# Optimization experiments

Hardware: AMD Instinct MI355X
Metric: run time of the kernel (lower is better)

The kernel has to match this reference:

```python
import jax, jax.numpy as jnp
import numpy as np
from functools import partial

N_NODES = 100000
N_EDGES = 3200000
F_IN, H1, H2, C_OUT = 128, 64, 32, 2


def setup_inputs() -> dict:
    key = jax.random.key(0)
    ks = jax.random.split(key, 8)
    x = jax.random.normal(ks[0], (N_NODES, F_IN), dtype=jnp.float32)
    edge_index = jax.random.randint(ks[1], (2, N_EDGES), 0, N_NODES, dtype=jnp.int64)
    def glorot(k, fan_in, fan_out):
        s = jnp.sqrt(6.0 / (fan_in + fan_out))
        return jax.random.uniform(k, (fan_in, fan_out), jnp.float32, -s, s)
    return {
        "x": x,
        "edge_index": edge_index,
        "W1": glorot(ks[2], F_IN, H1), "b1": jnp.zeros((H1,), jnp.float32),
        "W2": glorot(ks[3], H1, H2),   "b2": jnp.zeros((H2,), jnp.float32),
        "W3": glorot(ks[4], H2, C_OUT), "b3": jnp.zeros((C_OUT,), jnp.float32),
    }


def _gcn_norm(edge_index, num_nodes):
    # add self-loops, compute symmetric normalization D^{-1/2} (A+I) D^{-1/2}
    loop = jnp.arange(num_nodes, dtype=edge_index.dtype)
    src = jnp.concatenate([edge_index[0], loop])
    dst = jnp.concatenate([edge_index[1], loop])
    deg = jax.ops.segment_sum(jnp.ones_like(dst, dtype=jnp.float32), dst,
                              num_segments=num_nodes)
    dinv = jax.lax.rsqrt(deg)  # deg >= 1 because of self-loops
    norm = dinv[src] * dinv[dst]  # [E + N]
    return src, dst, norm


def _gcn_conv(x, W, b, src, dst, norm, num_nodes):
    # PyG GCNConv: linear transform, then normalized scatter-aggregate, then bias
    xw = x @ W                                   # [N, F_out]
    msg = xw[src] * norm[:, None]                # [E+N, F_out] gather + scale
    out = jax.ops.segment_sum(msg, dst, num_segments=num_nodes)
    return out + b


def reference(x, edge_index, W1, b1, W2, b2, W3, b3):
    n = x.shape[0]
    src, dst, norm = _gcn_norm(edge_index, n)
    h = jax.nn.relu(_gcn_conv(x, W1, b1, src, dst, norm, n))
    # dropout is identity in eval mode
    h = jax.nn.relu(_gcn_conv(h, W2, b2, src, dst, norm, n))
    h = _gcn_conv(h, W3, b3, src, dst, norm, n)
    return jax.nn.log_softmax(h, axis=1)
```

## Files before the change

### kernel.cpp

```cpp
#include <hip/hip_runtime.h>
#include <hip/hip_bf16.h>
#include <math.h>

constexpr int N = 100000;
constexpr int E = 3200000;
constexpr int FIN = 128, H1 = 64, H2 = 32, COUT = 2;

constexpr int BUK_SHIFT = 6;
constexpr int BUK_NODES = 64;
constexpr int NBUK = (N + BUK_NODES - 1) / BUK_NODES;
constexpr int CAP = 2560;
constexpr int SEG_SHIFT = 14;
constexpr int NSEG = 7;
constexpr int KEYS = BUK_NODES * NSEG;
constexpr int RP_STR = BUK_NODES + 1;

constexpr int MS_TPB = 1024;
constexpr int MS_EPT = 24;
constexpr int CHUNK = MS_TPB * MS_EPT;
constexpr int MS_WGS = (E + CHUNK - 1) / CHUNK;

__global__ void k_initcur(int* __restrict__ gcursor) {
    int i = blockIdx.x * blockDim.x + threadIdx.x;
    if (i < NBUK) gcursor[i] = i * CAP;
}

__global__ __launch_bounds__(MS_TPB)
void k_mslice(const int* __restrict__ src, const int* __restrict__ dst,
              int* __restrict__ gcursor, unsigned* __restrict__ ebuf) {
    __shared__ int cnt[NBUK];
    __shared__ int base[NBUK];
    const int t = threadIdx.x;
    for (int i = t; i < NBUK; i += MS_TPB) cnt[i] = 0;
    __syncthreads();
    const int e0 = blockIdx.x * CHUNK;

    int rb[MS_EPT];
    unsigned rv[MS_EPT];
#pragma unroll
    for (int j = 0; j < MS_EPT; ++j) {
        int e = e0 + j * MS_TPB + t;
        if (e < E) {
            int d = dst[e];
            int b = d >> BUK_SHIFT;
            rb[j] = b;
            rv[j] = (unsigned)src[e] | ((unsigned)(d & (BUK_NODES - 1)) << 17);
            atomicAdd(&cnt[b], 1);
        } else {
            rb[j] = -1; rv[j] = 0;
        }
    }
    __syncthreads();
    for (int i = t; i < NBUK; i += MS_TPB) {
        int c = cnt[i];
        base[i] = c ? atomicAdd(&gcursor[i], c) : 0;
    }
    __syncthreads();
    for (int i = t; i < NBUK; i += MS_TPB) cnt[i] = 0;
    __syncthreads();
#pragma unroll
    for (int j = 0; j < MS_EPT; ++j) {
        int b = rb[j];
        if (b >= 0) {
            int r = atomicAdd(&cnt[b], 1);
            int p = base[b] + r;
            if (p < (b + 1) * CAP) ebuf[p] = rv[j];
        }
    }
}

__global__ __launch_bounds__(256)
void k_build(const int* __restrict__ gcursor, unsigned* __restrict__ ebuf,
             int* __restrict__ rp, float* __restrict__ dinv) {
    __shared__ unsigned ent[CAP];
    __shared__ int cnt[512];
    __shared__ int sa[512];
    __shared__ int sb[512];
    __shared__ int cur[512];
    const int b = blockIdx.x;
    const int t = threadIdx.x;
    int fill = gcursor[b] - b * CAP;
    if (fill > CAP) fill = CAP;
    const int gbase = b * CAP;

    cnt[t] = 0; cnt[t + 256] = 0;
    __syncthreads();
    for (int j = t; j < fill; j += 256) {
        unsigned v = ebuf[gbase + j];
        ent[j] = v;
        int key = (int)(v >> 17) * NSEG + (int)((v & 0x1FFFFu) >> SEG_SHIFT);
        atomicAdd(&cnt[key], 1);
    }
    __syncthreads();
    sa[t] = cnt[t]; sa[t + 256] = cnt[t + 256];
    __syncthreads();
    int* pin = sa; int* pout = sb;
    for (int off = 1; off < 512; off <<= 1) {
        pout[t]       = pin[t]       + ((t >= off)       ? pin[t - off]       : 0);
        pout[t + 256] = pin[t + 256] + ((t + 256 >= off) ? pin[t + 256 - off] : 0);
        __syncthreads();
        int* tmp = pin; pin = pout; pout = tmp;
    }
    {
        int ex0 = pin[t] - cnt[t];
        int ex1 = pin[t + 256] - cnt[t + 256];
        cur[t] = gbase + ex0;
        cur[t + 256] = gbase + ex1;
        if (t < KEYS && (t % NSEG) == 0)
            rp[b * RP_STR + t / NSEG] = gbase + ex0;
        int k2 = t + 256;
        if (k2 < KEYS && (k2 % NSEG) == 0)
            rp[b * RP_STR + k2 / NSEG] = gbase + ex1;
        if (t == 0) rp[b * RP_STR + BUK_NODES] = gbase + fill;
    }
    if (t < BUK_NODES) {
        int deg = 0;
#pragma unroll
        for (int s = 0; s < NSEG; ++s) deg += cnt[t * NSEG + s];
        int node = (b << BUK_SHIFT) + t;
        if (node < N) dinv[node] = rsqrtf((float)deg + 1.0f);
    }
    __syncthreads();
    for (int j = t; j < fill; j += 256) {
        unsigned v = ent[j];
        int key = (int)(v >> 17) * NSEG + (int)((v & 0x1FFFFu) >> SEG_SHIFT);
        int p = atomicAdd(&cur[key], 1);
        ebuf[p] = v & 0x1FFFFu;
    }
}

template<int FI, int FO>
__global__ __launch_bounds__(256)
void k_gemm_tile_bf(const float* __restrict__ h, const float* __restrict__ Wg,
                    const float* __restrict__ dinv, __hip_bfloat16* __restrict__ y) {
    constexpr int TX  = FO / 4;
    constexpr int TY  = 256 / TX;
    constexpr int RPT = 64 / TY;
    constexpr int XS  = 68;
    constexpr int KQ  = FI / 4;

    __shared__ float xsT[FI][XS];

    const int tid = threadIdx.x;
    const int tx = tid % TX;
    const int ty = tid / TX;
    const int row0 = blockIdx.x * 64;

    for (int idx = tid; idx < 64 * KQ; idx += 256) {
        int g   = idx / 8;
        int rlo = idx % 8;
        int k4  = g % KQ;
        int rhi = g / KQ;
        int r   = rlo + 8 * rhi;
        int row = row0 + r;
        float4 v = make_float4(0.f, 0.f, 0.f, 0.f);
        if (row < N) v = *(const float4*)(h + (size_t)row * FI + 4 * k4);
        xsT[4 * k4 + 0][r] = v.x;
        xsT[4 * k4 + 1][r] = v.y;
        xsT[4 * k4 + 2][r] = v.z;
        xsT[4 * k4 + 3][r] = v.w;
    }
    __syncthreads();

    float acc[RPT][4];
#pragma unroll
    for (int i = 0; i < RPT; ++i)
#pragma unroll
        for (int c = 0; c < 4; ++c) acc[i][c] = 0.0f;

#pragma unroll 4
    for (int k = 0; k < FI; ++k) {
        const float4 wv = *(const float4*)(Wg + (size_t)k * FO + 4 * tx);
        float xv[RPT];
        if constexpr (RPT == 4) {
            float4 t = *(const float4*)&xsT[k][4 * ty];
            xv[0] = t.x; xv[1] = t.y; xv[2] = t.z; xv[3] = t.w;
        } else {
            float2 t = *(const float2*)&xsT[k][2 * ty];
            xv[0] = t.x; xv[1] = t.y;
        }
#pragma unroll
        for (int i = 0; i < RPT; ++i) {
            acc[i][0] = fmaf(xv[i], wv.x, acc[i][0]);
            acc[i][1] = fmaf(xv[i], wv.y, acc[i][1]);
            acc[i][2] = fmaf(xv[i], wv.z, acc[i][2]);
            acc[i][3] = fmaf(xv[i], wv.w, acc[i][3]);
        }
    }

#pragma unroll
    for (int i = 0; i < RPT; ++i) {
        int row = row0 + ty * RPT + i;
        if (row >= N) continue;
        float di = dinv[row];
        auto cvt = [](float f) -> unsigned short {
            __hip_bfloat16 b = __float2bfloat16(f);
            return *reinterpret_cast<unsigned short*>(&b);
        };
        ushort4 pk;
        pk.x = cvt(di * acc[i][0]);
        pk.y = cvt(di * acc[i][1]);
        pk.z = cvt(di * acc[i][2]);
        pk.w = cvt(di * acc[i][3]);
        *(ushort4*)&y[(size_t)row * FO + 4 * tx] = pk;
    }
}

template<int FI, int FO, int ROWS>
__global__ __launch_bounds__(FO * ROWS)
void k_gemm_scale(const float* __restrict__ h, const float* __restrict__ W,
                  const float* __restrict__ dinv, float* __restrict__ y) {
    __shared__ float xs[ROWS][FI];
    const int j = threadIdx.x;
    const int r = threadIdx.y;
    const int row0 = blockIdx.x * ROWS;
    const int tid = r * FO + j;
    constexpr int NT = FO * ROWS;
    for (int t = tid; t < ROWS * FI; t += NT) {
        int rr = t / FI, kk = t % FI;
        int row = row0 + rr;
        xs[rr][kk] = (row < N) ? h[(size_t)row * FI + kk] : 0.0f;
    }
    __syncthreads();
    const int row = row0 + r;
    if (row >= N) return;
    float acc = 0.0f;
#pragma unroll
    for (int k = 0; k < FI; ++k)
        acc = fmaf(xs[r][k], W[k * FO + j], acc);
    y[(size_t)row * FO + j] = dinv[row] * acc;
}

template<int F, bool RELU>
__global__ __launch_bounds__(256)
void k_aggregate_bf(const int* __restrict__ rp, const unsigned* __restrict__ csr,
                    const __hip_bfloat16* __restrict__ y, const float* __restrict__ dinv,
                    const float* __restrict__ b, float* __restrict__ out) {
    constexpr int LPN = F / 2;
    constexpr int NPB = 256 / LPN;
    const int fp = threadIdx.x;
    const int n = blockIdx.x * NPB + threadIdx.y;
    if (n >= N) return;
    const unsigned* yw = (const unsigned*)y;

    auto load2 = [&](int s) -> float2 {
        unsigned u = yw[(size_t)s * LPN + fp];
        float2 v;
        v.x = __uint_as_float(u << 16);
        v.y = __uint_as_float(u & 0xffff0000u);
        return v;
    };

    const int rb = (n >> BUK_SHIFT) * RP_STR + (n & (BUK_NODES - 1));
    const int j0 = rp[rb], j1 = rp[rb + 1];
    float2 acc = load2(n);
    int j = j0;
    for (; j + 8 <= j1; j += 8) {
        int s0 = (int)csr[j],     s1 = (int)csr[j + 1], s2 = (int)csr[j + 2], s3 = (int)csr[j + 3];
        int s4 = (int)csr[j + 4], s5 = (int)csr[j + 5], s6 = (int)csr[j + 6], s7 = (int)csr[j + 7];
        float2 v0 = load2(s0), v1 = load2(s1), v2 = load2(s2), v3 = load2(s3);
        float2 v4 = load2(s4), v5 = load2(s5), v6 = load2(s6), v7 = load2(s7);
        acc.x += ((v0.x + v1.x) + (v2.x + v3.x)) + ((v4.x + v5.x) + (v6.x + v7.x));
        acc.y += ((v0.y + v1.y) + (v2.y + v3.y)) + ((v4.y + v5.y) + (v6.y + v7.y));
    }
    for (; j < j1; ++j) {
        float2 v = load2((int)csr[j]);
        acc.x += v.x; acc.y += v.y;
    }
    const float di = dinv[n];
    float o0 = fmaf(di, acc.x, b[2 * fp]);
    float o1 = fmaf(di, acc.y, b[2 * fp + 1]);
    if (RELU) { o0 = fmaxf(o0, 0.0f); o1 = fmaxf(o1, 0.0f); }
    float2 res; res.x = o0; res.y = o1;
    *(float2*)&out[(size_t)n * F + 2 * fp] = res;
}

__global__ __launch_bounds__(256)
void k_final(const int* __restrict__ rp, const unsigned* __restrict__ csr,
             const float* __restrict__ y, const float* __restrict__ dinv,
             const float* __restrict__ bias, float* __restrict__ out) {
    const int c = threadIdx.x;
    const int n = blockIdx.x * 128 + threadIdx.y;
    float z = 0.0f;
    if (n < N) {
        const int rb = (n >> BUK_SHIFT) * RP_STR + (n & (BUK_NODES - 1));
        int j = rp[rb];
        const int j1 = rp[rb + 1];
        float acc = y[2 * n + c];
        for (; j + 4 <= j1; j += 4) {
            int s0 = (int)csr[j], s1 = (int)csr[j + 1], s2 = (int)csr[j + 2], s3 = (int)csr[j + 3];
            float a0 = y[2 * s0 + c], a1 = y[2 * s1 + c];
            float a2 = y[2 * s2 + c], a3 = y[2 * s3 + c];
            acc += (a0 + a1) + (a2 + a3);
        }
        for (; j < j1; ++j) acc += y[2 * (int)csr[j] + c];
        z = fmaf(dinv[n], acc, bias[c]);
    }
    float zo = __shfl_xor(z, 1);
    if (n < N) {
        float m = fmaxf(z, zo);
        float lse = m + logf(expf(z - m) + expf(zo - m));
        out[2 * n + c] = z - lse;
    }
}

extern "C" void kernel_launch(void* const* d_in, const int* in_sizes, int n_in,
                              void* d_out, int out_size, void* d_ws, size_t ws_size,
                              hipStream_t stream) {
    const float* x   = (const float*)d_in[0];
    const int*   ei  = (const int*)d_in[1];
    const float* W1  = (const float*)d_in[2];
    const float* b1  = (const float*)d_in[3];
    const float* W2  = (const float*)d_in[4];
    const float* b2  = (const float*)d_in[5];
    const float* W3  = (const float*)d_in[6];
    const float* b3  = (const float*)d_in[7];
    float* out = (float*)d_out;

    const int* src = ei;
    const int* dst = ei + E;

    char* p = (char*)d_ws;
    float*    dinv    = (float*)p;    p += (size_t)N * 4;
    int*      gcursor = (int*)p;      p += (size_t)NBUK * 4;
    int*      rp      = (int*)p;      p += (size_t)NBUK * RP_STR * 4;
    unsigned* ebuf    = (unsigned*)p; p += (size_t)NBUK * CAP * 4;
    char*     bufA    = p;            p += (size_t)N * 64 * 4;
    char*     bufB    = p;            p += (size_t)N * 64 * 4;

    __hip_bfloat16* y1 = (__hip_bfloat16*)bufA;
    float*          h1 = (float*)bufB;
    __hip_bfloat16* y2 = (__hip_bfloat16*)bufA;
    float*          h2 = (float*)(bufA + (size_t)N * H2 * 2);
    float*          y3 = (float*)bufB;

    k_initcur<<<(NBUK + 255) / 256, 256, 0, stream>>>(gcursor);
    k_mslice <<<MS_WGS, MS_TPB, 0, stream>>>(src, dst, gcursor, ebuf);
    k_build  <<<NBUK, 256, 0, stream>>>(gcursor, ebuf, rp, dinv);

    k_gemm_tile_bf<FIN, H1><<<(N + 63) / 64, 256, 0, stream>>>(x, W1, dinv, y1);
    k_aggregate_bf<H1, true><<<(N + 7) / 8, dim3(32, 8), 0, stream>>>(rp, ebuf, y1, dinv, b1, h1);

    k_gemm_tile_bf<H1, H2><<<(N + 63) / 64, 256, 0, stream>>>(h1, W2, dinv, y2);
    k_aggregate_bf<H2, true><<<(N + 15) / 16, dim3(16, 16), 0, stream>>>(rp, ebuf, y2, dinv, b2, h2);

    k_gemm_scale<H2, COUT, 128><<<(N + 127) / 128, dim3(COUT, 128), 0, stream>>>(h2, W3, dinv, y3);
    k_final<<<(N + 127) / 128, dim3(2, 128), 0, stream>>>(rp, ebuf, y3, dinv, b3, out);
}
```

Measured before the change: 379.2 us.

## Use persistent aggregation grids, finer source segments, and memset cursor init

The aggregation kernels now run as a fixed-size persistent grid that loops over node groups, replacing one block per group. The CSR build sorts each bucket's edges into 13 source segments of 8K nodes instead of 7 of 16K, which changes the gather order for better locality, and it widens the local histogram and scan to 1024 bins. The per-bucket cursor-initialization kernel is replaced by a memset, with cursors now relative offsets. The costs are a longer scan in the build step and the loop overhead of a grid-stride loop.

```diff
diff --git a/kernel.cpp b/kernel.cpp
--- a/kernel.cpp
+++ b/kernel.cpp
@@ -10,9 +10,10 @@
 constexpr int BUK_NODES = 64;
 constexpr int NBUK = (N + BUK_NODES - 1) / BUK_NODES;
 constexpr int CAP = 2560;
-constexpr int SEG_SHIFT = 14;
-constexpr int NSEG = 7;
+constexpr int SEG_SHIFT = 13;
+constexpr int NSEG = 13;
 constexpr int KEYS = BUK_NODES * NSEG;
+constexpr int BINS = 1024;
 constexpr int RP_STR = BUK_NODES + 1;
 
 constexpr int MS_TPB = 1024;
@@ -20,10 +21,7 @@
 constexpr int CHUNK = MS_TPB * MS_EPT;
 constexpr int MS_WGS = (E + CHUNK - 1) / CHUNK;
 
-__global__ void k_initcur(int* __restrict__ gcursor) {
-    int i = blockIdx.x * blockDim.x + threadIdx.x;
-    if (i < NBUK) gcursor[i] = i * CAP;
-}
+constexpr int PERS_BLKS = 1536;
 
 __global__ __launch_bounds__(MS_TPB)
 void k_mslice(const int* __restrict__ src, const int* __restrict__ dst,
@@ -64,7 +62,7 @@
         if (b >= 0) {
             int r = atomicAdd(&cnt[b], 1);
             int p = base[b] + r;
-            if (p < (b + 1) * CAP) ebuf[p] = rv[j];
+            if (p < CAP) ebuf[(size_t)b * CAP + p] = rv[j];
         }
     }
 }
@@ -73,17 +71,18 @@
 void k_build(const int* __restrict__ gcursor, unsigned* __restrict__ ebuf,
              int* __restrict__ rp, float* __restrict__ dinv) {
     __shared__ unsigned ent[CAP];
-    __shared__ int cnt[512];
-    __shared__ int sa[512];
-    __shared__ int sb[512];
-    __shared__ int cur[512];
+    __shared__ int cnt[BINS];
+    __shared__ int sa[BINS];
+    __shared__ int sb[BINS];
+    __shared__ int cur[BINS];
     const int b = blockIdx.x;
     const int t = threadIdx.x;
-    int fill = gcursor[b] - b * CAP;
+    int fill = gcursor[b];
     if (fill > CAP) fill = CAP;
     const int gbase = b * CAP;
 
-    cnt[t] = 0; cnt[t + 256] = 0;
+#pragma unroll
+    for (int q = 0; q < 4; ++q) cnt[t + 256 * q] = 0;
     __syncthreads();
     for (int j = t; j < fill; j += 256) {
         unsigned v = ebuf[gbase + j];
@@ -92,27 +91,28 @@
         atomicAdd(&cnt[key], 1);
     }
     __syncthreads();
-    sa[t] = cnt[t]; sa[t + 256] = cnt[t + 256];
+#pragma unroll
+    for (int q = 0; q < 4; ++q) sa[t + 256 * q] = cnt[t + 256 * q];
     __syncthreads();
     int* pin = sa; int* pout = sb;
-    for (int off = 1; off < 512; off <<= 1) {
-        pout[t]       = pin[t]       + ((t >= off)       ? pin[t - off]       : 0);
-        pout[t + 256] = pin[t + 256] + ((t + 256 >= off) ? pin[t + 256 - off] : 0);
+    for (int off = 1; off < BINS; off <<= 1) {
+#pragma unroll
+        for (int q = 0; q < 4; ++q) {
+            int idx = t + 256 * q;
+            pout[idx] = pin[idx] + ((idx >= off) ? pin[idx - off] : 0);
+        }
         __syncthreads();
         int* tmp = pin; pin = pout; pout = tmp;
     }
-    {
-        int ex0 = pin[t] - cnt[t];
-        int ex1 = pin[t + 256] - cnt[t + 256];
-        cur[t] = gbase + ex0;
-        cur[t + 256] = gbase + ex1;
-        if (t < KEYS && (t % NSEG) == 0)
-            rp[b * RP_STR + t / NSEG] = gbase + ex0;
-        int k2 = t + 256;
-        if (k2 < KEYS && (k2 % NSEG) == 0)
-            rp[b * RP_STR + k2 / NSEG] = gbase + ex1;
-        if (t == 0) rp[b * RP_STR + BUK_NODES] = gbase + fill;
-    }
+#pragma unroll
+    for (int q = 0; q < 4; ++q) {
+        int idx = t + 256 * q;
+        int ex = pin[idx] - cnt[idx];
+        cur[idx] = gbase + ex;
+        if (idx < KEYS && (idx % NSEG) == 0)
+            rp[b * RP_STR + idx / NSEG] = gbase + ex;
+    }
+    if (t == 0) rp[b * RP_STR + BUK_NODES] = gbase + fill;
     if (t < BUK_NODES) {
         int deg = 0;
 #pragma unroll
@@ -238,9 +238,8 @@
                     const float* __restrict__ b, float* __restrict__ out) {
     constexpr int LPN = F / 2;
     constexpr int NPB = 256 / LPN;
+    constexpr int NGRP = (N + NPB - 1) / NPB;
     const int fp = threadIdx.x;
-    const int n = blockIdx.x * NPB + threadIdx.y;
-    if (n >= N) return;
     const unsigned* yw = (const unsigned*)y;
 
     auto load2 = [&](int s) -> float2 {
@@ -251,28 +250,32 @@
         return v;
     };
 
-    const int rb = (n >> BUK_SHIFT) * RP_STR + (n & (BUK_NODES - 1));
-    const int j0 = rp[rb], j1 = rp[rb + 1];
-    float2 acc = load2(n);
-    int j = j0;
-    for (; j + 8 <= j1; j += 8) {
-        int s0 = (int)csr[j],     s1 = (int)csr[j + 1], s2 = (int)csr[j + 2], s3 = (int)csr[j + 3];
-        int s4 = (int)csr[j + 4], s5 = (int)csr[j + 5], s6 = (int)csr[j + 6], s7 = (int)csr[j + 7];
-        float2 v0 = load2(s0), v1 = load2(s1), v2 = load2(s2), v3 = load2(s3);
-        float2 v4 = load2(s4), v5 = load2(s5), v6 = load2(s6), v7 = load2(s7);
-        acc.x += ((v0.x + v1.x) + (v2.x + v3.x)) + ((v4.x + v5.x) + (v6.x + v7.x));
-        acc.y += ((v0.y + v1.y) + (v2.y + v3.y)) + ((v4.y + v5.y) + (v6.y + v7.y));
-    }
-    for (; j < j1; ++j) {
-        float2 v = load2((int)csr[j]);
-        acc.x += v.x; acc.y += v.y;
-    }
-    const float di = dinv[n];
-    float o0 = fmaf(di, acc.x, b[2 * fp]);
-    float o1 = fmaf(di, acc.y, b[2 * fp + 1]);
-    if (RELU) { o0 = fmaxf(o0, 0.0f); o1 = fmaxf(o1, 0.0f); }
-    float2 res; res.x = o0; res.y = o1;
-    *(float2*)&out[(size_t)n * F + 2 * fp] = res;
+    for (int g = blockIdx.x; g < NGRP; g += gridDim.x) {
+        const int n = g * NPB + threadIdx.y;
+        if (n >= N) continue;
+        const int rb = (n >> BUK_SHIFT) * RP_STR + (n & (BUK_NODES - 1));
+        const int j0 = rp[rb], j1 = rp[rb + 1];
+        float2 acc = load2(n);
+        int j = j0;
+        for (; j + 8 <= j1; j += 8) {
+            int s0 = (int)csr[j],     s1 = (int)csr[j + 1], s2 = (int)csr[j + 2], s3 = (int)csr[j + 3];
+            int s4 = (int)csr[j + 4], s5 = (int)csr[j + 5], s6 = (int)csr[j + 6], s7 = (int)csr[j + 7];
+            float2 v0 = load2(s0), v1 = load2(s1), v2 = load2(s2), v3 = load2(s3);
+            float2 v4 = load2(s4), v5 = load2(s5), v6 = load2(s6), v7 = load2(s7);
+            acc.x += ((v0.x + v1.x) + (v2.x + v3.x)) + ((v4.x + v5.x) + (v6.x + v7.x));
+            acc.y += ((v0.y + v1.y) + (v2.y + v3.y)) + ((v4.y + v5.y) + (v6.y + v7.y));
+        }
+        for (; j < j1; ++j) {
+            float2 v = load2((int)csr[j]);
+            acc.x += v.x; acc.y += v.y;
+        }
+        const float di = dinv[n];
+        float o0 = fmaf(di, acc.x, b[2 * fp]);
+        float o1 = fmaf(di, acc.y, b[2 * fp + 1]);
+        if (RELU) { o0 = fmaxf(o0, 0.0f); o1 = fmaxf(o1, 0.0f); }
+        float2 res; res.x = o0; res.y = o1;
+        *(float2*)&out[(size_t)n * F + 2 * fp] = res;
+    }
 }
 
 __global__ __launch_bounds__(256)
@@ -334,15 +337,15 @@
     float*          h2 = (float*)(bufA + (size_t)N * H2 * 2);
     float*          y3 = (float*)bufB;
 
-    k_initcur<<<(NBUK + 255) / 256, 256, 0, stream>>>(gcursor);
-    k_mslice <<<MS_WGS, MS_TPB, 0, stream>>>(src, dst, gcursor, ebuf);
-    k_build  <<<NBUK, 256, 0, stream>>>(gcursor, ebuf, rp, dinv);
+    hipMemsetAsync(gcursor, 0, (size_t)NBUK * 4, stream);
+    k_mslice<<<MS_WGS, MS_TPB, 0, stream>>>(src, dst, gcursor, ebuf);
+    k_build <<<NBUK, 256, 0, stream>>>(gcursor, ebuf, rp, dinv);
 
     k_gemm_tile_bf<FIN, H1><<<(N + 63) / 64, 256, 0, stream>>>(x, W1, dinv, y1);
-    k_aggregate_bf<H1, true><<<(N + 7) / 8, dim3(32, 8), 0, stream>>>(rp, ebuf, y1, dinv, b1, h1);
+    k_aggregate_bf<H1, true><<<PERS_BLKS, dim3(32, 8), 0, stream>>>(rp, ebuf, y1, dinv, b1, h1);
 
     k_gemm_tile_bf<H1, H2><<<(N + 63) / 64, 256, 0, stream>>>(h1, W2, dinv, y2);
-    k_aggregate_bf<H2, true><<<(N + 15) / 16, dim3(16, 16), 0, stream>>>(rp, ebuf, y2, dinv, b2, h2);
+    k_aggregate_bf<H2, true><<<PERS_BLKS, dim3(16, 16), 0, stream>>>(rp, ebuf, y2, dinv, b2, h2);
 
     k_gemm_scale<H2, COUT, 128><<<(N + 127) / 128, dim3(COUT, 128), 0, stream>>>(h2, W3, dinv, y3);
     k_final<<<(N + 127) / 128, dim3(2, 128), 0, stream>>>(rp, ebuf, y3, dinv, b3, out);
```

Measured after the change: 404.5 us. 6.7% more time.
